# Kernel tuning notes

Hardware: AMD Instinct MI355X
Metric: run time of the kernel (lower is better)

## Reference

```python
import jax, jax.numpy as jnp
import numpy as np

N_NODES = 50000
N_EDGES = 800000
IN_CH = 128
HID = 128


def setup_inputs() -> dict:
    key = jax.random.key(0)
    ks = jax.random.split(key, 16)
    inp = {
        "x": jax.random.normal(ks[0], (N_NODES, IN_CH), dtype=jnp.float32),
        "edge_index": jax.random.randint(ks[1], (2, N_EDGES), 0, N_NODES, dtype=jnp.int64),
        "batch_size": 1024,
    }
    dims = [(IN_CH, HID), (HID, HID), (HID, HID)]
    for i, (din, dout) in enumerate(dims):
        s = 1.0 / np.sqrt(din)
        inp[f"W_l{i}"] = jax.random.uniform(ks[2 + 4 * i], (dout, din), jnp.float32, -s, s)
        inp[f"b_l{i}"] = jax.random.uniform(ks[3 + 4 * i], (dout,), jnp.float32, -s, s)
        inp[f"W_r{i}"] = jax.random.uniform(ks[4 + 4 * i], (dout, din), jnp.float32, -s, s)
        inp[f"a{i}"] = jnp.full((dout,), 0.25, dtype=jnp.float32)  # PReLU slope
    return inp


def _sage_prelu(x, src, dst, W_l, b_l, W_r, a):
    # mean aggregation of source messages at target nodes
    msg_sum = jax.ops.segment_sum(x[src], dst, num_segments=N_NODES)  # [N, din]
    deg = jax.ops.segment_sum(jnp.ones((src.shape[0],), x.dtype), dst, num_segments=N_NODES)
    agg = msg_sum / jnp.maximum(deg, 1.0)[:, None]
    out = agg @ W_l.T + b_l + x @ W_r.T  # lin_l(aggr) + lin_r(x), bias on lin_l only
    return jnp.where(out > 0, out, a * out)  # per-channel PReLU


def reference(x, edge_index, batch_size, W_l0, b_l0, W_r0, a0, W_l1, b_l1, W_r1, a1, W_l2, b_l2, W_r2, a2):
    src, dst = edge_index[0], edge_index[1]
    x = _sage_prelu(x, src, dst, W_l0, b_l0, W_r0, a0)
    x = _sage_prelu(x, src, dst, W_l1, b_l1, W_r1, a1)
    x = _sage_prelu(x, src, dst, W_l2, b_l2, W_r2, a2)
    return x[:batch_size]
```

## Files before the change

kernel.cpp:

```cpp
#include <hip/hip_runtime.h>

#define NN 50000
#define NE 800000
#define C 128
#define CAP 64
#define EB2 ((NE / 2 + 255) / 256)
#define SPLITB 1563
#define WB 96
#define MB4 ((NE / 4 + 255) / 256)
#define EB4 ((NE / 4 + 255) / 256)
#define CB  ((NN + 255) / 256)
#define ASTRIDE 136

typedef __attribute__((ext_vector_type(8))) short bf16x8;
typedef __attribute__((ext_vector_type(4))) float f32x4;
typedef unsigned short ushort;

__device__ inline ushort bf16_rn(float f) {
    unsigned u = __builtin_bit_cast(unsigned, f);
    u += 0x7FFF + ((u >> 16) & 1);
    return (ushort)(u >> 16);
}
__device__ inline void split_bf16(float f, ushort& hi, ushort& lo) {
    hi = bf16_rn(f);
    float hif = __builtin_bit_cast(float, (unsigned)hi << 16);
    lo = bf16_rn(f - hif);
}
__device__ inline float bf_lo(unsigned u) { return __builtin_bit_cast(float, u << 16); }
__device__ inline float bf_hi(unsigned u) { return __builtin_bit_cast(float, u & 0xFFFF0000u); }


__global__ __launch_bounds__(256)
void prep_kernel(const int* __restrict__ src, const int* __restrict__ dst,
                 const float* __restrict__ x,
                 const float* __restrict__ W0, const float* __restrict__ W1,
                 const float* __restrict__ W2, const float* __restrict__ W3,
                 const float* __restrict__ W4, const float* __restrict__ W5,
                 int* __restrict__ deg, int* __restrict__ pos,
                 ushort* __restrict__ Ah, ushort* __restrict__ Al,
                 ushort* __restrict__ Wh, ushort* __restrict__ Wl,
                 int* __restrict__ needed, int rows_out) {
    int t = threadIdx.x;
    if (blockIdx.x < EB2) {
        int e0 = (blockIdx.x * 256 + t) * 2;
        if (e0 < NE) {
            int2 d2 = *(const int2*)(dst + e0);
            int p0 = atomicAdd(&deg[d2.x], 1);
            int p1 = atomicAdd(&deg[d2.y], 1);
            *(int2*)(pos + e0) = make_int2(p0, p1);
        }
    } else if (blockIdx.x < EB2 + SPLITB) {
        int tid = (blockIdx.x - EB2) * 256 + t;
        const int total = NN * C / 4;
        for (int i = tid; i < total; i += SPLITB * 256) {
            f32x4 v = ((const f32x4*)x)[i];
            ushort h0, h1, h2, h3, l0, l1, l2, l3;
            split_bf16(v.x, h0, l0);
            split_bf16(v.y, h1, l1);
            split_bf16(v.z, h2, l2);
            split_bf16(v.w, h3, l3);
            *(uint2*)(Ah + (size_t)i * 4) = make_uint2((unsigned)h0 | ((unsigned)h1 << 16),
                                                       (unsigned)h2 | ((unsigned)h3 << 16));
            *(uint2*)(Al + (size_t)i * 4) = make_uint2((unsigned)l0 | ((unsigned)l1 << 16),
                                                       (unsigned)l2 | ((unsigned)l3 << 16));
        }
    } else if (blockIdx.x < EB2 + SPLITB + WB) {
        const float* Ws[6] = {W0, W1, W2, W3, W4, W5};
        int i = (blockIdx.x - EB2 - SPLITB) * 256 + t;
        int mat = i >> 12;
        f32x4 v = ((const f32x4*)Ws[mat])[i & 4095];
        ushort h0, h1, h2, h3, l0, l1, l2, l3;
        split_bf16(v.x, h0, l0);
        split_bf16(v.y, h1, l1);
        split_bf16(v.z, h2, l2);
        split_bf16(v.w, h3, l3);
        *(uint2*)(Wh + (size_t)i * 4) = make_uint2((unsigned)h0 | ((unsigned)h1 << 16),
                                                   (unsigned)h2 | ((unsigned)h3 << 16));
        *(uint2*)(Wl + (size_t)i * 4) = make_uint2((unsigned)l0 | ((unsigned)l1 << 16),
                                                   (unsigned)l2 | ((unsigned)l3 << 16));
    } else {
        int e0 = ((blockIdx.x - EB2 - SPLITB - WB) * 256 + t) * 4;
        if (e0 < NE) {
            int4 da = *(const int4*)(dst + e0);
            int4 sa = *(const int4*)(src + e0);
            if (da.x < rows_out) needed[sa.x] = 1;
            if (da.y < rows_out) needed[sa.y] = 1;
            if (da.z < rows_out) needed[sa.z] = 1;
            if (da.w < rows_out) needed[sa.w] = 1;
        }
    }
}


__global__ __launch_bounds__(256)
void fill_kernel(const int* __restrict__ src, const int* __restrict__ dst,
                 const int* __restrict__ pos, int* __restrict__ col,
                 const int* __restrict__ needed, int* __restrict__ list,
                 int* __restrict__ cnt, int rows_out) {
    int t = threadIdx.x;
    if (blockIdx.x < EB4) {
        int e0 = (blockIdx.x * 256 + t) * 4;
        if (e0 >= NE) return;
        int4 da = *(const int4*)(dst + e0);
        int4 sa = *(const int4*)(src + e0);
        int4 pa = *(const int4*)(pos + e0);
        if (pa.x < CAP) col[da.x * CAP + pa.x] = sa.x;
        if (pa.y < CAP) col[da.y * CAP + pa.y] = sa.y;
        if (pa.z < CAP) col[da.z * CAP + pa.z] = sa.z;
        if (pa.w < CAP) col[da.w * CAP + pa.w] = sa.w;
    } else {
        int i = (blockIdx.x - EB4) * 256 + t;
        if (i < NN && (i < rows_out || needed[i])) {
            int p = atomicAdd(cnt, 1);
            list[p] = i;
        }
    }
}


__global__ __launch_bounds__(256)
void agg_kernel(const ushort* __restrict__ xh, const int* __restrict__ deg,
                const int* __restrict__ col,
                const int* __restrict__ list, const int* __restrict__ countp,
                ushort* __restrict__ aggh, ushort* __restrict__ aggl, int nodes) {
    int i = (blockIdx.x * blockDim.x + threadIdx.x) >> 6;
    int lane = threadIdx.x & 63;
    int cnt = list ? *countp : nodes;
    if (i >= cnt) return;
    int node = list ? list[i] : i;
    int quad = lane >> 4;
    int ql   = lane & 15;
    int d = min(deg[node], CAP);
    int start = node * CAP;
    int end = start + d;
    const uint4* xr = (const uint4*)xh;
    float a0=0,a1=0,a2=0,a3=0,a4=0,a5=0,a6=0,a7=0;
    int e = start;
    for (; e + 7 < end; e += 8) {
        int i0 = col[e + quad];
        int i1 = col[e + 4 + quad];
        uint4 u0 = xr[(size_t)i0 * 16 + ql];
        uint4 u1 = xr[(size_t)i1 * 16 + ql];
        a0 += bf_lo(u0.x) + bf_lo(u1.x); a1 += bf_hi(u0.x) + bf_hi(u1.x);
        a2 += bf_lo(u0.y) + bf_lo(u1.y); a3 += bf_hi(u0.y) + bf_hi(u1.y);
        a4 += bf_lo(u0.z) + bf_lo(u1.z); a5 += bf_hi(u0.z) + bf_hi(u1.z);
        a6 += bf_lo(u0.w) + bf_lo(u1.w); a7 += bf_hi(u0.w) + bf_hi(u1.w);
    }
    for (; e + 3 < end; e += 4) {
        uint4 u = xr[(size_t)col[e + quad] * 16 + ql];
        a0 += bf_lo(u.x); a1 += bf_hi(u.x);
        a2 += bf_lo(u.y); a3 += bf_hi(u.y);
        a4 += bf_lo(u.z); a5 += bf_hi(u.z);
        a6 += bf_lo(u.w); a7 += bf_hi(u.w);
    }
    int rem = end - e;
    if (quad < rem) {
        uint4 u = xr[(size_t)col[e + quad] * 16 + ql];
        a0 += bf_lo(u.x); a1 += bf_hi(u.x);
        a2 += bf_lo(u.y); a3 += bf_hi(u.y);
        a4 += bf_lo(u.z); a5 += bf_hi(u.z);
        a6 += bf_lo(u.w); a7 += bf_hi(u.w);
    }
    a0 += __shfl_xor(a0, 16, 64); a0 += __shfl_xor(a0, 32, 64);
    a1 += __shfl_xor(a1, 16, 64); a1 += __shfl_xor(a1, 32, 64);
    a2 += __shfl_xor(a2, 16, 64); a2 += __shfl_xor(a2, 32, 64);
    a3 += __shfl_xor(a3, 16, 64); a3 += __shfl_xor(a3, 32, 64);
    a4 += __shfl_xor(a4, 16, 64); a4 += __shfl_xor(a4, 32, 64);
    a5 += __shfl_xor(a5, 16, 64); a5 += __shfl_xor(a5, 32, 64);
    a6 += __shfl_xor(a6, 16, 64); a6 += __shfl_xor(a6, 32, 64);
    a7 += __shfl_xor(a7, 16, 64); a7 += __shfl_xor(a7, 32, 64);
    if (quad == 0) {
        float inv = 1.0f / (float)max(d, 1);
        float m[8] = {a0*inv, a1*inv, a2*inv, a3*inv, a4*inv, a5*inv, a6*inv, a7*inv};
        ushort h[8], o[8];
        #pragma unroll
        for (int j = 0; j < 8; ++j) split_bf16(m[j], h[j], o[j]);
        size_t off = (size_t)node * C + ql * 8;
        *(uint4*)(aggh + off) = make_uint4((unsigned)h[0] | ((unsigned)h[1] << 16),
                                           (unsigned)h[2] | ((unsigned)h[3] << 16),
                                           (unsigned)h[4] | ((unsigned)h[5] << 16),
                                           (unsigned)h[6] | ((unsigned)h[7] << 16));
        *(uint4*)(aggl + off) = make_uint4((unsigned)o[0] | ((unsigned)o[1] << 16),
                                           (unsigned)o[2] | ((unsigned)o[3] << 16),
                                           (unsigned)o[4] | ((unsigned)o[5] << 16),
                                           (unsigned)o[6] | ((unsigned)o[7] << 16));
    }
}


__global__ __launch_bounds__(256, 4)
void gemm_kernel(const ushort* __restrict__ Ah, const ushort* __restrict__ Al,
                 const ushort* __restrict__ Xh, const ushort* __restrict__ Xl,
                 const ushort* __restrict__ Wlh, const ushort* __restrict__ Wll,
                 const ushort* __restrict__ Wrh, const ushort* __restrict__ Wrl,
                 const float* __restrict__ bl, const float* __restrict__ slope,
                 const int* __restrict__ list, const int* __restrict__ countp,
                 float* __restrict__ outf, ushort* __restrict__ outh,
                 ushort* __restrict__ outl, int rows) {
    __shared__ ushort Ahi[64 * ASTRIDE];
    __shared__ ushort Alo[64 * ASTRIDE];
    int t = threadIdx.x;
    int lane = t & 63;
    int w = t >> 6;
    int l = lane & 15;
    int q = lane >> 4;
    int row0 = blockIdx.x * 64;
    int cnt = list ? min(*countp, rows) : rows;
    if (row0 >= cnt) return;

    f32x4 acc[4][2];
    #pragma unroll
    for (int mt = 0; mt < 4; ++mt)
        #pragma unroll
        for (int nt = 0; nt < 2; ++nt)
            acc[mt][nt] = (f32x4){0.f, 0.f, 0.f, 0.f};

    #pragma unroll
    for (int mat = 0; mat < 2; ++mat) {
        const ushort* WH = mat ? Wrh : Wlh;
        const ushort* WL = mat ? Wrl : Wll;
        const ushort* Ph = mat ? Xh : Ah;
        const ushort* Pl = mat ? Xl : Al;

        bf16x8 bhi[2][4], blo[2][4];
        #pragma unroll
        for (int nt = 0; nt < 2; ++nt) {
            int n = w * 32 + nt * 16 + l;
            const ushort* wp = WH + (size_t)n * C + q * 8;
            const ushort* wq = WL + (size_t)n * C + q * 8;
            #pragma unroll
            for (int kb = 0; kb < 4; ++kb) {
                bhi[nt][kb] = *(const bf16x8*)(wp + kb * 32);
                blo[nt][kb] = *(const bf16x8*)(wq + kb * 32);
            }
        }

        __syncthreads();
        int ar = t >> 2;
        int aq = t & 3;
        int ridx = min(row0 + ar, cnt - 1);
        int r = list ? list[ridx] : ridx;
        ushort* dh = Ahi + ar * ASTRIDE + aq * 32;
        ushort* dl = Alo + ar * ASTRIDE + aq * 32;
        const ushort* ph = Ph + (size_t)r * C + aq * 32;
        const ushort* pl = Pl + (size_t)r * C + aq * 32;
        #pragma unroll
        for (int i = 0; i < 4; ++i) {
            *(uint4*)(dh + i * 8) = *(const uint4*)(ph + i * 8);
            *(uint4*)(dl + i * 8) = *(const uint4*)(pl + i * 8);
        }
        __syncthreads();

        #pragma unroll
        for (int kb = 0; kb < 4; ++kb) {
            #pragma unroll
            for (int mt = 0; mt < 4; ++mt) {
                int off = (mt * 16 + l) * ASTRIDE + kb * 32 + q * 8;
                bf16x8 ahi = *(const bf16x8*)(Ahi + off);
                bf16x8 alo = *(const bf16x8*)(Alo + off);
                #pragma unroll
                for (int nt = 0; nt < 2; ++nt) {
                    acc[mt][nt] = __builtin_amdgcn_mfma_f32_16x16x32_bf16(ahi, bhi[nt][kb], acc[mt][nt], 0, 0, 0);
                    acc[mt][nt] = __builtin_amdgcn_mfma_f32_16x16x32_bf16(alo, bhi[nt][kb], acc[mt][nt], 0, 0, 0);
                    acc[mt][nt] = __builtin_amdgcn_mfma_f32_16x16x32_bf16(ahi, blo[nt][kb], acc[mt][nt], 0, 0, 0);
                }
            }
        }
    }

    #pragma unroll
    for (int nt = 0; nt < 2; ++nt) {
        int n = w * 32 + nt * 16 + l;
        float b = bl[n], s = slope[n];
        #pragma unroll
        for (int mt = 0; mt < 4; ++mt) {
            #pragma unroll
            for (int rg = 0; rg < 4; ++rg) {
                int ridx = row0 + mt * 16 + q * 4 + rg;
                if (ridx < cnt) {
                    int r = list ? list[ridx] : ridx;
                    float v = acc[mt][nt][rg] + b;
                    v = v > 0.f ? v : s * v;
                    if (outf) {
                        outf[(size_t)r * C + n] = v;
                    } else {
                        ushort hh, ll;
                        split_bf16(v, hh, ll);
                        outh[(size_t)r * C + n] = hh;
                        outl[(size_t)r * C + n] = ll;
                    }
                }
            }
        }
    }
}


extern "C" void kernel_launch(void* const* d_in, const int* in_sizes, int n_in,
                              void* d_out, int out_size, void* d_ws, size_t ws_size,
                              hipStream_t stream) {
    const float* x   = (const float*)d_in[0];
    const int*   src = (const int*)d_in[1];
    const int*   dst = src + NE;
    const float* Wl[3] = {(const float*)d_in[3], (const float*)d_in[7],  (const float*)d_in[11]};
    const float* bl[3] = {(const float*)d_in[4], (const float*)d_in[8],  (const float*)d_in[12]};
    const float* Wr[3] = {(const float*)d_in[5], (const float*)d_in[9],  (const float*)d_in[13]};
    const float* sl[3] = {(const float*)d_in[6], (const float*)d_in[10], (const float*)d_in[14]};

    int*   deg     = (int*)d_ws;
    int*   needed  = deg + 50016;
    int*   cnt     = needed + 50016;
    int*   pos     = cnt + 16;
    int*   col     = pos + 800000;
    int*   list    = col + NN * CAP;
    ushort* Whs    = (ushort*)(list + 50016);
    ushort* Wls    = Whs + 6 * 16384;
    ushort* Gh     = Wls + 6 * 16384;
    ushort* Gl     = Gh + (size_t)NN * C;
    ushort* Ah     = Gl + (size_t)NN * C;
    ushort* Al     = Ah + (size_t)NN * C;
    ushort* Bh     = Al + (size_t)NN * C;
    ushort* Bl     = Bh + (size_t)NN * C;

    int rows_out = out_size / C;

    hipMemsetAsync(deg, 0, (2 * 50016 + 16) * sizeof(int), stream);

    prep_kernel<<<EB2 + SPLITB + WB + MB4, 256, 0, stream>>>(
        src, dst, x, Wl[0], Wr[0], Wl[1], Wr[1], Wl[2], Wr[2],
        deg, pos, Ah, Al, Whs, Wls, needed, rows_out);
    fill_kernel<<<EB4 + CB, 256, 0, stream>>>(src, dst, pos, col, needed, list, cnt, rows_out);

    agg_kernel<<<(NN + 3) / 4, 256, 0, stream>>>(Ah, deg, col, nullptr, nullptr, Gh, Gl, NN);
    gemm_kernel<<<(NN + 63) / 64, 256, 0, stream>>>(Gh, Gl, Ah, Al,
                                                    Whs + 0 * 16384, Wls + 0 * 16384,
                                                    Whs + 1 * 16384, Wls + 1 * 16384,
                                                    bl[0], sl[0], nullptr, nullptr,
                                                    nullptr, Bh, Bl, NN);

    agg_kernel<<<(NN + 3) / 4, 256, 0, stream>>>(Bh, deg, col, list, cnt, Gh, Gl, NN);
    gemm_kernel<<<(NN + 63) / 64, 256, 0, stream>>>(Gh, Gl, Bh, Bl,
                                                    Whs + 2 * 16384, Wls + 2 * 16384,
                                                    Whs + 3 * 16384, Wls + 3 * 16384,
                                                    bl[1], sl[1], list, cnt,
                                                    nullptr, Ah, Al, NN);

    agg_kernel<<<(rows_out + 3) / 4, 256, 0, stream>>>(Ah, deg, col, nullptr, nullptr,
                                                       Gh, Gl, rows_out);
    gemm_kernel<<<(rows_out + 63) / 64, 256, 0, stream>>>(Gh, Gl, Ah, Al,
                                                          Whs + 4 * 16384, Wls + 4 * 16384,
                                                          Whs + 5 * 16384, Wls + 5 * 16384,
                                                          bl[2], sl[2], nullptr, nullptr,
                                                          (float*)d_out, nullptr, nullptr,
                                                          rows_out);
}
```

Baseline: 287.4 us.

## Fuse CSR fill into degree pass and fold list build into first aggregation

The degree-counting pass now writes source indices straight into the fixed-capacity adjacency slots using the atomic return value, and also marks needed nodes. This removes the intermediate pos array and the separate fill kernel. The compaction of needed nodes into a work list moves into extra blocks of the first aggregation launch, which saves one kernel launch and the pos round trip through memory. The cost is that the col scatter writes now sit behind the atomics in the same threads.

```diff
diff --git a/kernel.cpp b/kernel.cpp
--- a/kernel.cpp
+++ b/kernel.cpp
@@ -4,12 +4,11 @@
 #define NE 800000
 #define C 128
 #define CAP 64
-#define EB2 ((NE / 2 + 255) / 256)
+#define EP4 ((NE / 4 + 255) / 256)
 #define SPLITB 1563
 #define WB 96
-#define MB4 ((NE / 4 + 255) / 256)
-#define EB4 ((NE / 4 + 255) / 256)
 #define CB  ((NN + 255) / 256)
+#define AGG0B ((NN + 3) / 4)
 #define ASTRIDE 136
 
 typedef __attribute__((ext_vector_type(8))) short bf16x8;
@@ -36,21 +35,31 @@
                  const float* __restrict__ W0, const float* __restrict__ W1,
                  const float* __restrict__ W2, const float* __restrict__ W3,
                  const float* __restrict__ W4, const float* __restrict__ W5,
-                 int* __restrict__ deg, int* __restrict__ pos,
+                 int* __restrict__ deg, int* __restrict__ col,
                  ushort* __restrict__ Ah, ushort* __restrict__ Al,
                  ushort* __restrict__ Wh, ushort* __restrict__ Wl,
                  int* __restrict__ needed, int rows_out) {
     int t = threadIdx.x;
-    if (blockIdx.x < EB2) {
-        int e0 = (blockIdx.x * 256 + t) * 2;
+    if (blockIdx.x < EP4) {
+        int e0 = (blockIdx.x * 256 + t) * 4;
         if (e0 < NE) {
-            int2 d2 = *(const int2*)(dst + e0);
-            int p0 = atomicAdd(&deg[d2.x], 1);
-            int p1 = atomicAdd(&deg[d2.y], 1);
-            *(int2*)(pos + e0) = make_int2(p0, p1);
-        }
-    } else if (blockIdx.x < EB2 + SPLITB) {
-        int tid = (blockIdx.x - EB2) * 256 + t;
+            int4 da = *(const int4*)(dst + e0);
+            int4 sa = *(const int4*)(src + e0);
+            int p0 = atomicAdd(&deg[da.x], 1);
+            int p1 = atomicAdd(&deg[da.y], 1);
+            int p2 = atomicAdd(&deg[da.z], 1);
+            int p3 = atomicAdd(&deg[da.w], 1);
+            if (p0 < CAP) col[da.x * CAP + p0] = sa.x;
+            if (p1 < CAP) col[da.y * CAP + p1] = sa.y;
+            if (p2 < CAP) col[da.z * CAP + p2] = sa.z;
+            if (p3 < CAP) col[da.w * CAP + p3] = sa.w;
+            if (da.x < rows_out) needed[sa.x] = 1;
+            if (da.y < rows_out) needed[sa.y] = 1;
+            if (da.z < rows_out) needed[sa.z] = 1;
+            if (da.w < rows_out) needed[sa.w] = 1;
+        }
+    } else if (blockIdx.x < EP4 + SPLITB) {
+        int tid = (blockIdx.x - EP4) * 256 + t;
         const int total = NN * C / 4;
         for (int i = tid; i < total; i += SPLITB * 256) {
             f32x4 v = ((const f32x4*)x)[i];
@@ -64,9 +73,9 @@
             *(uint2*)(Al + (size_t)i * 4) = make_uint2((unsigned)l0 | ((unsigned)l1 << 16),
                                                        (unsigned)l2 | ((unsigned)l3 << 16));
         }
-    } else if (blockIdx.x < EB2 + SPLITB + WB) {
+    } else {
         const float* Ws[6] = {W0, W1, W2, W3, W4, W5};
-        int i = (blockIdx.x - EB2 - SPLITB) * 256 + t;
+        int i = (blockIdx.x - EP4 - SPLITB) * 256 + t;
         int mat = i >> 12;
         f32x4 v = ((const f32x4*)Ws[mat])[i & 4095];
         ushort h0, h1, h2, h3, l0, l1, l2, l3;
@@ -78,42 +87,6 @@
                                                    (unsigned)h2 | ((unsigned)h3 << 16));
         *(uint2*)(Wl + (size_t)i * 4) = make_uint2((unsigned)l0 | ((unsigned)l1 << 16),
                                                    (unsigned)l2 | ((unsigned)l3 << 16));
-    } else {
-        int e0 = ((blockIdx.x - EB2 - SPLITB - WB) * 256 + t) * 4;
-        if (e0 < NE) {
-            int4 da = *(const int4*)(dst + e0);
-            int4 sa = *(const int4*)(src + e0);
-            if (da.x < rows_out) needed[sa.x] = 1;
-            if (da.y < rows_out) needed[sa.y] = 1;
-            if (da.z < rows_out) needed[sa.z] = 1;
-            if (da.w < rows_out) needed[sa.w] = 1;
-        }
-    }
-}
-
-
-__global__ __launch_bounds__(256)
-void fill_kernel(const int* __restrict__ src, const int* __restrict__ dst,
-                 const int* __restrict__ pos, int* __restrict__ col,
-                 const int* __restrict__ needed, int* __restrict__ list,
-                 int* __restrict__ cnt, int rows_out) {
-    int t = threadIdx.x;
-    if (blockIdx.x < EB4) {
-        int e0 = (blockIdx.x * 256 + t) * 4;
-        if (e0 >= NE) return;
-        int4 da = *(const int4*)(dst + e0);
-        int4 sa = *(const int4*)(src + e0);
-        int4 pa = *(const int4*)(pos + e0);
-        if (pa.x < CAP) col[da.x * CAP + pa.x] = sa.x;
-        if (pa.y < CAP) col[da.y * CAP + pa.y] = sa.y;
-        if (pa.z < CAP) col[da.z * CAP + pa.z] = sa.z;
-        if (pa.w < CAP) col[da.w * CAP + pa.w] = sa.w;
-    } else {
-        int i = (blockIdx.x - EB4) * 256 + t;
-        if (i < NN && (i < rows_out || needed[i])) {
-            int p = atomicAdd(cnt, 1);
-            list[p] = i;
-        }
     }
 }
 
@@ -122,7 +95,17 @@
 void agg_kernel(const ushort* __restrict__ xh, const int* __restrict__ deg,
                 const int* __restrict__ col,
                 const int* __restrict__ list, const int* __restrict__ countp,
-                ushort* __restrict__ aggh, ushort* __restrict__ aggl, int nodes) {
+                ushort* __restrict__ aggh, ushort* __restrict__ aggl, int nodes,
+                int aggblocks, const int* __restrict__ needed,
+                int* __restrict__ wlist, int* __restrict__ wcnt, int rows_out) {
+    if (needed && blockIdx.x >= aggblocks) {
+        int i = (blockIdx.x - aggblocks) * 256 + threadIdx.x;
+        if (i < NN && (i < rows_out || needed[i])) {
+            int p = atomicAdd(wcnt, 1);
+            wlist[p] = i;
+        }
+        return;
+    }
     int i = (blockIdx.x * blockDim.x + threadIdx.x) >> 6;
     int lane = threadIdx.x & 63;
     int cnt = list ? *countp : nodes;
@@ -310,8 +293,7 @@
     int*   deg     = (int*)d_ws;
     int*   needed  = deg + 50016;
     int*   cnt     = needed + 50016;
-    int*   pos     = cnt + 16;
-    int*   col     = pos + 800000;
+    int*   col     = cnt + 16;
     int*   list    = col + NN * CAP;
     ushort* Whs    = (ushort*)(list + 50016);
     ushort* Wls    = Whs + 6 * 16384;
@@ -326,19 +308,20 @@
 
     hipMemsetAsync(deg, 0, (2 * 50016 + 16) * sizeof(int), stream);
 
-    prep_kernel<<<EB2 + SPLITB + WB + MB4, 256, 0, stream>>>(
+    prep_kernel<<<EP4 + SPLITB + WB, 256, 0, stream>>>(
         src, dst, x, Wl[0], Wr[0], Wl[1], Wr[1], Wl[2], Wr[2],
-        deg, pos, Ah, Al, Whs, Wls, needed, rows_out);
-    fill_kernel<<<EB4 + CB, 256, 0, stream>>>(src, dst, pos, col, needed, list, cnt, rows_out);
-
-    agg_kernel<<<(NN + 3) / 4, 256, 0, stream>>>(Ah, deg, col, nullptr, nullptr, Gh, Gl, NN);
+        deg, col, Ah, Al, Whs, Wls, needed, rows_out);
+
+    agg_kernel<<<AGG0B + CB, 256, 0, stream>>>(Ah, deg, col, nullptr, nullptr, Gh, Gl, NN,
+                                               AGG0B, needed, list, cnt, rows_out);
     gemm_kernel<<<(NN + 63) / 64, 256, 0, stream>>>(Gh, Gl, Ah, Al,
                                                     Whs + 0 * 16384, Wls + 0 * 16384,
                                                     Whs + 1 * 16384, Wls + 1 * 16384,
                                                     bl[0], sl[0], nullptr, nullptr,
                                                     nullptr, Bh, Bl, NN);
 
-    agg_kernel<<<(NN + 3) / 4, 256, 0, stream>>>(Bh, deg, col, list, cnt, Gh, Gl, NN);
+    agg_kernel<<<AGG0B, 256, 0, stream>>>(Bh, deg, col, list, cnt, Gh, Gl, NN,
+                                          AGG0B, nullptr, nullptr, nullptr, rows_out);
     gemm_kernel<<<(NN + 63) / 64, 256, 0, stream>>>(Gh, Gl, Bh, Bl,
                                                     Whs + 2 * 16384, Wls + 2 * 16384,
                                                     Whs + 3 * 16384, Wls + 3 * 16384,
@@ -346,7 +329,9 @@
                                                     nullptr, Ah, Al, NN);
 
     agg_kernel<<<(rows_out + 3) / 4, 256, 0, stream>>>(Ah, deg, col, nullptr, nullptr,
-                                                       Gh, Gl, rows_out);
+                                                       Gh, Gl, rows_out,
+                                                       (rows_out + 3) / 4, nullptr,
+                                                       nullptr, nullptr, rows_out);
     gemm_kernel<<<(rows_out + 63) / 64, 256, 0, stream>>>(Gh, Gl, Ah, Al,
                                                           Whs + 4 * 16384, Wls + 4 * 16384,
                                                           Whs + 5 * 16384, Wls + 5 * 16384,
```

New measurement: 292.0 us. Within noise of the previous version (+1.6%).
